# Kernel optimization log

Measured on AMD Instinct MI355X. Metric: run time of the kernel, lower is better.

Reference implementation:

```python
import jax, jax.numpy as jnp
import numpy as np

B, T, D, H = 2, 2048, 2048, 16
HD = D // H  # head_dim = 128
ROPE_THETA = 10000.0


def _apply_rope_interleaved(x, cos, sin):
    # x: (B, T, H, HD); cos/sin: (1, T, 1, HD//2). rope_fraction=1.0, HD even.
    x1 = x[..., ::2]
    x2 = x[..., 1::2]
    rot = jnp.stack([x1 * cos - x2 * sin, x1 * sin + x2 * cos], axis=-1)
    return rot.reshape(x.shape)


def setup_inputs() -> dict:
    key = jax.random.key(0)
    k1, k2, k3 = jax.random.split(key, 3)
    x = jax.random.normal(k1, (B, T, D), dtype=jnp.float32)
    # DenseGeneral qkv kernel: (D, H, 3*HD), lecun_normal-ish scale
    w_qkv = jax.random.normal(k2, (D, H, 3 * HD), dtype=jnp.float32) / np.sqrt(D)
    # out Dense kernel: (D, D)
    w_out = jax.random.normal(k3, (D, D), dtype=jnp.float32) / np.sqrt(D)
    return {"x": x, "w_qkv": w_qkv, "w_out": w_out}


def reference(x, w_qkv, w_out):
    # Fused QKV projection: (B,T,D) x (D,H,3HD) -> (B,T,H,3HD)
    qkv = jnp.einsum("btd,dhf->bthf", x, w_qkv)
    q, k, v = jnp.split(qkv, 3, axis=-1)  # each (B,T,H,HD)

    # RoPE cos/sin at positions arange(T)
    pos = jnp.arange(T, dtype=jnp.float32)
    inv_freq = 1.0 / (ROPE_THETA ** (jnp.arange(0, HD, 2, dtype=jnp.float32) / HD))
    angles = pos[:, None] * inv_freq[None, :]  # (T, HD//2)
    cos = jnp.cos(angles)[None, :, None, :]
    sin = jnp.sin(angles)[None, :, None, :]

    q = _apply_rope_interleaved(q, cos, sin)
    k = _apply_rope_interleaved(k, cos, sin)

    sm_scale = 1.0 / np.sqrt(HD)
    # (B,H,T,HD)
    qh = jnp.transpose(q, (0, 2, 1, 3))
    kh = jnp.transpose(k, (0, 2, 1, 3))
    vh = jnp.transpose(v, (0, 2, 1, 3))

    scores = jnp.einsum("bhqd,bhkd->bhqk", qh, kh) * sm_scale
    causal = jnp.tril(jnp.ones((T, T), dtype=bool))
    scores = jnp.where(causal[None, None], scores, jnp.float32(-1e30))
    probs = jax.nn.softmax(scores, axis=-1)
    yh = jnp.einsum("bhqk,bhkd->bhqd", probs, vh)

    y = jnp.transpose(yh, (0, 2, 1, 3)).reshape(B, T, D)
    # deterministic=True -> dropout is identity; out projection
    return jnp.einsum("btd,de->bte", y, w_out)
```

## Files before the change

kernel.cpp:

```cpp
#include <hip/hip_runtime.h>
#include <math.h>

typedef unsigned short u16;
typedef unsigned int u32;
typedef __attribute__((ext_vector_type(8))) short short8;
typedef __attribute__((ext_vector_type(4))) float f32x4;

#define Bb 2
#define Tt 2048
#define Dd 2048
#define Hh 16
#define HDim 128
#define NQKV 6144

__device__ __forceinline__ u16 f2b(float f) {
    u32 u = __float_as_uint(f);
    u32 r = (u + 0x7FFFu + ((u >> 16) & 1u)) >> 16;
    return (u16)r;
}
__device__ __forceinline__ float2 b2f2(u32 u) {
    return make_float2(__uint_as_float(u << 16), __uint_as_float(u & 0xFFFF0000u));
}
__device__ __forceinline__ u32 pack2(float a, float b) {
    return (u32)f2b(a) | ((u32)f2b(b) << 16);
}

__global__ __launch_bounds__(256) void cast_f32_bf16(const float* __restrict__ src,
                                                     u16* __restrict__ dst, int n) {
    int i = (blockIdx.x * 256 + threadIdx.x) * 4;
    if (i >= n) return;
    float4 v = *(const float4*)(src + i);
    *(uint2*)(dst + i) = make_uint2(pack2(v.x, v.y), pack2(v.z, v.w));
}

__global__ __launch_bounds__(256) void transpose_cast(const float* __restrict__ src,
                                                      u16* __restrict__ dst, int R, int C) {
    __shared__ float tile[32][33];
    int c0 = blockIdx.x << 5, r0 = blockIdx.y << 5;
    int tx = threadIdx.x & 31, ty = threadIdx.x >> 5;
    #pragma unroll
    for (int i = 0; i < 32; i += 8)
        tile[ty + i][tx] = src[(size_t)(r0 + ty + i) * C + c0 + tx];
    __syncthreads();
    #pragma unroll
    for (int i = 0; i < 32; i += 8)
        dst[(size_t)(c0 + ty + i) * R + r0 + tx] = f2b(tile[tx][ty + i]);
}

template <bool F32OUT>
__global__ __launch_bounds__(256) void gemm_bt(const u16* __restrict__ A, const u16* __restrict__ Bt,
                                               void* __restrict__ Cv, int Mn, int Nn, int Kn) {
    __shared__ __align__(16) u16 As[128 * 40];
    __shared__ __align__(16) u16 Bs[128 * 40];
    const int tid = threadIdx.x;
    const int m0 = blockIdx.y << 7, n0 = blockIdx.x << 7;
    const int wave = tid >> 6, lane = tid & 63;
    const int wm = (wave >> 1) << 6, wn = (wave & 1) << 6;
    const int l15 = lane & 15, lq = lane >> 4;

    f32x4 acc[4][4];
    #pragma unroll
    for (int i = 0; i < 4; i++)
        #pragma unroll
        for (int j = 0; j < 4; j++)
            acc[i][j] = (f32x4){0.f, 0.f, 0.f, 0.f};

    const int r1 = tid >> 2;
    const int c1 = (tid & 3) << 3;

    for (int k0 = 0; k0 < Kn; k0 += 32) {
        __syncthreads();
        #pragma unroll
        for (int i = 0; i < 2; i++) {
            int row = r1 + (i << 6);
            *(uint4*)&As[row * 40 + c1] = *(const uint4*)(A + (size_t)(m0 + row) * Kn + k0 + c1);
            *(uint4*)&Bs[row * 40 + c1] = *(const uint4*)(Bt + (size_t)(n0 + row) * Kn + k0 + c1);
        }
        __syncthreads();
        short8 a[4], b[4];
        #pragma unroll
        for (int i = 0; i < 4; i++) {
            a[i] = *(const short8*)&As[(wm + (i << 4) + l15) * 40 + lq * 8];
            b[i] = *(const short8*)&Bs[(wn + (i << 4) + l15) * 40 + lq * 8];
        }
        #pragma unroll
        for (int i = 0; i < 4; i++)
            #pragma unroll
            for (int j = 0; j < 4; j++)
                acc[i][j] = __builtin_amdgcn_mfma_f32_16x16x32_bf16(a[i], b[j], acc[i][j], 0, 0, 0);
    }

    #pragma unroll
    for (int i = 0; i < 4; i++) {
        int mbase = m0 + wm + (i << 4) + (lq << 2);
        #pragma unroll
        for (int j = 0; j < 4; j++) {
            int n = n0 + wn + (j << 4) + l15;
            #pragma unroll
            for (int r = 0; r < 4; r++) {
                if constexpr (F32OUT)
                    ((float*)Cv)[(size_t)(mbase + r) * Nn + n] = acc[i][j][r];
                else
                    ((u16*)Cv)[(size_t)(mbase + r) * Nn + n] = f2b(acc[i][j][r]);
            }
        }
    }
}

__global__ __launch_bounds__(256) void rope_reorder(const u16* __restrict__ qkv, u16* __restrict__ qh,
                                                    u16* __restrict__ kh, u16* __restrict__ vh) {
    int gid = blockIdx.x * 256 + threadIdx.x;
    int i = gid & 63;
    int t = (gid >> 6) & 2047;
    int h = (gid >> 17) & 15;
    int b = gid >> 21;
    const u16* src = qkv + ((size_t)(b * Tt + t)) * NQKV + h * 384;
    u32 uq = *(const u32*)(src + 2 * i);
    u32 uk = *(const u32*)(src + 128 + 2 * i);
    u32 uv = *(const u32*)(src + 256 + 2 * i);
    float ang = (float)t * exp2f(-0.20762050596f * (float)i);
    float sv, cv;
    sincosf(ang, &sv, &cv);
    float2 q = b2f2(uq), k = b2f2(uk);
    size_t o = ((size_t)(b * Hh + h) * Tt + t) * HDim + 2 * i;
    *(u32*)(qh + o) = pack2(q.x * cv - q.y * sv, q.x * sv + q.y * cv);
    *(u32*)(kh + o) = pack2(k.x * cv - k.y * sv, k.x * sv + k.y * cv);
    *(u32*)(vh + o) = uv;
}

#define KS 136
#define VTS 72

__global__ __launch_bounds__(512) void attn_mfma(const u16* __restrict__ qh, const u16* __restrict__ kh,
                                                 const u16* __restrict__ vh, u16* __restrict__ yb) {
    __shared__ __align__(16) u16 smem[17920];
    u16* Qs = smem;
    u16* Ks = smem;
    u16* Vt = smem + 8704;

    const int tid = threadIdx.x;
    const int bh = blockIdx.y;
    const int w = tid >> 6, lane = tid & 63;
    const int l15 = lane & 15, qa = lane >> 4;
    const u16* qp = qh + (size_t)bh * Tt * HDim;
    const u16* kp = kh + (size_t)bh * Tt * HDim;
    const u16* vp = vh + (size_t)bh * Tt * HDim;
    const int b = bh >> 4, h = bh & 15;
    const float CEXP = (float)(0.08838834764831845 * 1.4426950408889634);

    for (int pass = 0; pass < 2; pass++) {
        const int qt = pass ? (15 - (int)blockIdx.x) : (int)blockIdx.x;
        const int qbase = qt * 128 + w * 16;

        __syncthreads();
        #pragma unroll
        for (int i = 0; i < 4; i++) {
            int slot = tid + (i << 9);
            int row = slot >> 4, cb = slot & 15;
            *(uint4*)&Qs[row * KS + cb * 8] =
                *(const uint4*)(qp + (size_t)(qt * 128 + row) * HDim + cb * 8);
        }
        __syncthreads();
        short8 qfrag[4];
        #pragma unroll
        for (int dc = 0; dc < 4; dc++)
            qfrag[dc] = *(const short8*)&Qs[(w * 16 + l15) * KS + dc * 32 + qa * 8];

        float m2 = -1e30f, l_i = 0.f;
        f32x4 oacc[8];
        #pragma unroll
        for (int nt = 0; nt < 8; nt++) oacc[nt] = (f32x4){0.f, 0.f, 0.f, 0.f};

        const int nkt = 2 * qt + 2;
        for (int kt = 0; kt < nkt; kt++) {
            const int k0 = kt << 6;
            __syncthreads();
            #pragma unroll
            for (int i = 0; i < 2; i++) {
                int slot = tid + (i << 9);
                int row = slot >> 4, cb = slot & 15;
                *(uint4*)&Ks[row * KS + cb * 8] =
                    *(const uint4*)(kp + (size_t)(k0 + row) * HDim + cb * 8);
            }
            {
                int k = tid & 63;
                #pragma unroll
                for (int it = 0; it < 2; it++) {
                    int d0 = ((tid >> 6) << 3) + (it << 6);
                    uint4 vv = *(const uint4*)(vp + (size_t)(k0 + k) * HDim + d0);
                    const u16* pe = (const u16*)&vv;
                    #pragma unroll
                    for (int j = 0; j < 8; j++) Vt[(d0 + j) * VTS + k] = pe[j];
                }
            }
            __syncthreads();

            if (k0 <= qbase + 15) {
                float s2[4][4];
                #pragma unroll
                for (int mt = 0; mt < 4; mt++) {
                    f32x4 st = (f32x4){0.f, 0.f, 0.f, 0.f};
                    #pragma unroll
                    for (int dc = 0; dc < 4; dc++) {
                        short8 ka = *(const short8*)&Ks[(mt * 16 + l15) * KS + dc * 32 + qa * 8];
                        st = __builtin_amdgcn_mfma_f32_16x16x32_bf16(ka, qfrag[dc], st, 0, 0, 0);
                    }
                    #pragma unroll
                    for (int r = 0; r < 4; r++) s2[mt][r] = st[r] * CEXP;
                }
                if (k0 + 63 > qbase) {
                    int qg = qbase + l15;
                    #pragma unroll
                    for (int mt = 0; mt < 4; mt++)
                        #pragma unroll
                        for (int r = 0; r < 4; r++)
                            if (k0 + mt * 16 + qa * 4 + r > qg) s2[mt][r] = -1e30f;
                }
                float mx = m2;
                #pragma unroll
                for (int mt = 0; mt < 4; mt++)
                    #pragma unroll
                    for (int r = 0; r < 4; r++) mx = fmaxf(mx, s2[mt][r]);
                mx = fmaxf(mx, __shfl_xor(mx, 16, 64));
                mx = fmaxf(mx, __shfl_xor(mx, 32, 64));
                float alpha = exp2f(m2 - mx);
                m2 = mx;
                float rsum = 0.f;
                float p[4][4];
                #pragma unroll
                for (int mt = 0; mt < 4; mt++)
                    #pragma unroll
                    for (int r = 0; r < 4; r++) {
                        p[mt][r] = exp2f(s2[mt][r] - mx);
                        rsum += p[mt][r];
                    }
                rsum += __shfl_xor(rsum, 16, 64);
                rsum += __shfl_xor(rsum, 32, 64);
                l_i = l_i * alpha + rsum;
                float aO[4];
                #pragma unroll
                for (int r = 0; r < 4; r++) aO[r] = __shfl(alpha, qa * 4 + r, 64);
                #pragma unroll
                for (int nt = 0; nt < 8; nt++)
                    #pragma unroll
                    for (int r = 0; r < 4; r++) oacc[nt][r] *= aO[r];

                u32 pu[4][2];
                #pragma unroll
                for (int mt = 0; mt < 4; mt++) {
                    pu[mt][0] = pack2(p[mt][0], p[mt][1]);
                    pu[mt][1] = pack2(p[mt][2], p[mt][3]);
                }
                short8 pa[2];
                const int srcA = ((qa & 1) << 5) + l15;
                const int srcB = srcA + 16;
                #pragma unroll
                for (int c = 0; c < 2; c++) {
                    u32 A0 = __shfl((int)pu[2 * c][0], srcA, 64);
                    u32 A1 = __shfl((int)pu[2 * c][1], srcA, 64);
                    u32 A2 = __shfl((int)pu[2 * c][0], srcB, 64);
                    u32 A3 = __shfl((int)pu[2 * c][1], srcB, 64);
                    u32 B0 = __shfl((int)pu[2 * c + 1][0], srcA, 64);
                    u32 B1 = __shfl((int)pu[2 * c + 1][1], srcA, 64);
                    u32 B2 = __shfl((int)pu[2 * c + 1][0], srcB, 64);
                    u32 B3 = __shfl((int)pu[2 * c + 1][1], srcB, 64);
                    u32 wv[4];
                    wv[0] = (qa & 2) ? B0 : A0;
                    wv[1] = (qa & 2) ? B1 : A1;
                    wv[2] = (qa & 2) ? B2 : A2;
                    wv[3] = (qa & 2) ? B3 : A3;
                    pa[c] = *(short8*)wv;
                }
                #pragma unroll
                for (int nt = 0; nt < 8; nt++) {
                    short8 vb0 = *(const short8*)&Vt[(nt * 16 + l15) * VTS + qa * 8];
                    short8 vb1 = *(const short8*)&Vt[(nt * 16 + l15) * VTS + 32 + qa * 8];
                    oacc[nt] = __builtin_amdgcn_mfma_f32_16x16x32_bf16(pa[0], vb0, oacc[nt], 0, 0, 0);
                    oacc[nt] = __builtin_amdgcn_mfma_f32_16x16x32_bf16(pa[1], vb1, oacc[nt], 0, 0, 0);
                }
            }
        }

        float linv = 1.0f / l_i;
        float lr[4];
        #pragma unroll
        for (int r = 0; r < 4; r++) lr[r] = __shfl(linv, qa * 4 + r, 64);
        #pragma unroll
        for (int r = 0; r < 4; r++) {
            int t = qbase + qa * 4 + r;
            u16* dst = yb + ((size_t)(b * Tt + t)) * Dd + h * HDim + l15;
            #pragma unroll
            for (int nt = 0; nt < 8; nt++)
                dst[nt * 16] = f2b(oacc[nt][r] * lr[r]);
        }
    }
}

extern "C" void kernel_launch(void* const* d_in, const int* in_sizes, int n_in,
                              void* d_out, int out_size, void* d_ws, size_t ws_size,
                              hipStream_t stream) {
    const float* x     = (const float*)d_in[0];
    const float* w_qkv = (const float*)d_in[1];
    const float* w_out = (const float*)d_in[2];
    float* out = (float*)d_out;

    u16* ws    = (u16*)d_ws;
    u16* xb    = ws;
    u16* wqkvT = xb + 8388608;
    u16* woutT = wqkvT + 12582912;
    u16* qkvb  = woutT + 4194304;
    u16* qhb   = qkvb + 25165824;
    u16* khb   = qhb + 8388608;
    u16* vhb   = khb + 8388608;
    u16* yb    = vhb + 8388608;

    cast_f32_bf16<<<8192, 256, 0, stream>>>(x, xb, 8388608);
    transpose_cast<<<dim3(192, 64), 256, 0, stream>>>(w_qkv, wqkvT, 2048, 6144);
    transpose_cast<<<dim3(64, 64), 256, 0, stream>>>(w_out, woutT, 2048, 2048);
    gemm_bt<false><<<dim3(48, 32), 256, 0, stream>>>(xb, wqkvT, (void*)qkvb, 4096, 6144, 2048);
    rope_reorder<<<16384, 256, 0, stream>>>(qkvb, qhb, khb, vhb);
    attn_mfma<<<dim3(8, 32), 512, 0, stream>>>(qhb, khb, vhb, yb);
    gemm_bt<true><<<dim3(16, 32), 256, 0, stream>>>(yb, woutT, (void*)out, 4096, 2048, 2048);
}
```

Baseline: 454.0 us.

## Use direct global-to-LDS loads in GEMM and scatter QKV into head-major layout

The GEMM tile loads now use global_load_lds to write 16-byte chunks straight into unpadded shared memory, skipping the register round trip. The QKV GEMM epilogue scatters its outputs directly into planar per-head Q/K/V buffers. This removes the intermediate qkv buffer and lets RoPE run in place on Q and K only, without also copying V. The trade-off is that the unpadded LDS layout may cause bank conflicts on the fragment reads, and the epilogue's scattered 2-byte stores may coalesce less well.

```diff
diff --git a/kernel.cpp b/kernel.cpp
--- a/kernel.cpp
+++ b/kernel.cpp
@@ -24,6 +24,10 @@
 __device__ __forceinline__ u32 pack2(float a, float b) {
     return (u32)f2b(a) | ((u32)f2b(b) << 16);
 }
+
+#define GLD16(g, l) __builtin_amdgcn_global_load_lds(                                   \
+    (const __attribute__((address_space(1))) void*)(g),                                 \
+    (__attribute__((address_space(3))) void*)(l), 16, 0, 0)
 
 __global__ __launch_bounds__(256) void cast_f32_bf16(const float* __restrict__ src,
                                                      u16* __restrict__ dst, int n) {
@@ -47,11 +51,11 @@
         dst[(size_t)(c0 + ty + i) * R + r0 + tx] = f2b(tile[tx][ty + i]);
 }
 
-template <bool F32OUT>
+template <int OMODE>
 __global__ __launch_bounds__(256) void gemm_bt(const u16* __restrict__ A, const u16* __restrict__ Bt,
                                                void* __restrict__ Cv, int Mn, int Nn, int Kn) {
-    __shared__ __align__(16) u16 As[128 * 40];
-    __shared__ __align__(16) u16 Bs[128 * 40];
+    __shared__ __align__(16) u16 As[128 * 32];
+    __shared__ __align__(16) u16 Bs[128 * 32];
     const int tid = threadIdx.x;
     const int m0 = blockIdx.y << 7, n0 = blockIdx.x << 7;
     const int wave = tid >> 6, lane = tid & 63;
@@ -65,23 +69,25 @@
         for (int j = 0; j < 4; j++)
             acc[i][j] = (f32x4){0.f, 0.f, 0.f, 0.f};
 
-    const int r1 = tid >> 2;
-    const int c1 = (tid & 3) << 3;
+    const int srow = wave * 32 + (lane >> 2);
+    const int scol = (lane & 3) << 3;
+    const u16* ga = A + (size_t)(m0 + srow) * Kn + scol;
+    const u16* gb = Bt + (size_t)(n0 + srow) * Kn + scol;
+    u16* lA = &As[wave * 1024];
+    u16* lB = &Bs[wave * 1024];
 
     for (int k0 = 0; k0 < Kn; k0 += 32) {
         __syncthreads();
-        #pragma unroll
-        for (int i = 0; i < 2; i++) {
-            int row = r1 + (i << 6);
-            *(uint4*)&As[row * 40 + c1] = *(const uint4*)(A + (size_t)(m0 + row) * Kn + k0 + c1);
-            *(uint4*)&Bs[row * 40 + c1] = *(const uint4*)(Bt + (size_t)(n0 + row) * Kn + k0 + c1);
-        }
+        GLD16(ga + k0, lA);
+        GLD16(ga + k0 + (size_t)16 * Kn, lA + 512);
+        GLD16(gb + k0, lB);
+        GLD16(gb + k0 + (size_t)16 * Kn, lB + 512);
         __syncthreads();
         short8 a[4], b[4];
         #pragma unroll
         for (int i = 0; i < 4; i++) {
-            a[i] = *(const short8*)&As[(wm + (i << 4) + l15) * 40 + lq * 8];
-            b[i] = *(const short8*)&Bs[(wn + (i << 4) + l15) * 40 + lq * 8];
+            a[i] = *(const short8*)&As[(wm + (i << 4) + l15) * 32 + lq * 8];
+            b[i] = *(const short8*)&Bs[(wn + (i << 4) + l15) * 32 + lq * 8];
         }
         #pragma unroll
         for (int i = 0; i < 4; i++)
@@ -96,36 +102,37 @@
         #pragma unroll
         for (int j = 0; j < 4; j++) {
             int n = n0 + wn + (j << 4) + l15;
-            #pragma unroll
-            for (int r = 0; r < 4; r++) {
-                if constexpr (F32OUT)
+            if constexpr (OMODE == 1) {
+                #pragma unroll
+                for (int r = 0; r < 4; r++)
                     ((float*)Cv)[(size_t)(mbase + r) * Nn + n] = acc[i][j][r];
-                else
-                    ((u16*)Cv)[(size_t)(mbase + r) * Nn + n] = f2b(acc[i][j][r]);
+            } else {
+                int f = n >> 7;
+                int h = f / 3, sel = f - 3 * h;
+                int d = n & 127;
+                u16* base = (u16*)Cv + (size_t)sel * 8388608;
+                #pragma unroll
+                for (int r = 0; r < 4; r++) {
+                    int m = mbase + r;
+                    int b = m >> 11, t = m & 2047;
+                    base[(((size_t)(b * 16 + h)) * 2048 + t) * 128 + d] = f2b(acc[i][j][r]);
+                }
             }
         }
     }
 }
 
-__global__ __launch_bounds__(256) void rope_reorder(const u16* __restrict__ qkv, u16* __restrict__ qh,
-                                                    u16* __restrict__ kh, u16* __restrict__ vh) {
+__global__ __launch_bounds__(256) void rope_planar(u16* __restrict__ qk) {
     int gid = blockIdx.x * 256 + threadIdx.x;
     int i = gid & 63;
     int t = (gid >> 6) & 2047;
-    int h = (gid >> 17) & 15;
-    int b = gid >> 21;
-    const u16* src = qkv + ((size_t)(b * Tt + t)) * NQKV + h * 384;
-    u32 uq = *(const u32*)(src + 2 * i);
-    u32 uk = *(const u32*)(src + 128 + 2 * i);
-    u32 uv = *(const u32*)(src + 256 + 2 * i);
+    int bhz = gid >> 17;
+    u16* p = qk + ((size_t)bhz * 2048 + t) * 128 + 2 * i;
     float ang = (float)t * exp2f(-0.20762050596f * (float)i);
     float sv, cv;
     sincosf(ang, &sv, &cv);
-    float2 q = b2f2(uq), k = b2f2(uk);
-    size_t o = ((size_t)(b * Hh + h) * Tt + t) * HDim + 2 * i;
-    *(u32*)(qh + o) = pack2(q.x * cv - q.y * sv, q.x * sv + q.y * cv);
-    *(u32*)(kh + o) = pack2(k.x * cv - k.y * sv, k.x * sv + k.y * cv);
-    *(u32*)(vh + o) = uv;
+    float2 xy = b2f2(*(const u32*)p);
+    *(u32*)p = pack2(xy.x * cv - xy.y * sv, xy.x * sv + xy.y * cv);
 }
 
 #define KS 136
@@ -308,8 +315,7 @@
     u16* xb    = ws;
     u16* wqkvT = xb + 8388608;
     u16* woutT = wqkvT + 12582912;
-    u16* qkvb  = woutT + 4194304;
-    u16* qhb   = qkvb + 25165824;
+    u16* qhb   = woutT + 4194304;
     u16* khb   = qhb + 8388608;
     u16* vhb   = khb + 8388608;
     u16* yb    = vhb + 8388608;
@@ -317,8 +323,8 @@
     cast_f32_bf16<<<8192, 256, 0, stream>>>(x, xb, 8388608);
     transpose_cast<<<dim3(192, 64), 256, 0, stream>>>(w_qkv, wqkvT, 2048, 6144);
     transpose_cast<<<dim3(64, 64), 256, 0, stream>>>(w_out, woutT, 2048, 2048);
-    gemm_bt<false><<<dim3(48, 32), 256, 0, stream>>>(xb, wqkvT, (void*)qkvb, 4096, 6144, 2048);
-    rope_reorder<<<16384, 256, 0, stream>>>(qkvb, qhb, khb, vhb);
+    gemm_bt<2><<<dim3(48, 32), 256, 0, stream>>>(xb, wqkvT, (void*)qhb, 4096, 6144, 2048);
+    rope_planar<<<32768, 256, 0, stream>>>(qhb);
     attn_mfma<<<dim3(8, 32), 512, 0, stream>>>(qhb, khb, vhb, yb);
-    gemm_bt<true><<<dim3(16, 32), 256, 0, stream>>>(yb, woutT, (void*)out, 4096, 2048, 2048);
-}
+    gemm_bt<1><<<dim3(16, 32), 256, 0, stream>>>(yb, woutT, (void*)out, 4096, 2048, 2048);
+}
```

After: 442.8 us. 1.03x faster.
